# Kernel tuning notes

Hardware: AMD Instinct MI355X
Metric: run time of the kernel (lower is better)

The kernel has to match this reference:

```python
import jax, jax.numpy as jnp
import numpy as np

B, T, D = 4, 4096, 4096
G, C, K, M = 1, 4, 128, 32          # num_groups, n_splits, dw_hidden_dim, heads_per_group
I2 = 4                               # qkw inner dim = 2 * dynamic_hidden_dim (dyn_hidden = 32//16 = 2)
EPS = 1.1920929e-07                  # torch F.rms_norm default eps for fp32


def _rms_norm(x):
    # F.rms_norm over last dim, no learned scale
    return x * jax.lax.rsqrt(jnp.mean(x * x, axis=-1, keepdims=True) + EPS)


def setup_inputs() -> dict:
    key = jax.random.key(0)
    k0, k1, k2, k3 = jax.random.split(key, 4)
    dw1_std = np.sqrt(2.0 / (D + K))
    qkw_std = 0.02 / (np.sqrt(2 * 32 * 2) * (32 + 2))
    dd_std = 0.05 * np.sqrt(2.0 / (32 + D))
    return {
        "query_vec": jax.random.normal(k0, (B, T, D), dtype=jnp.float32),
        "dw1": jax.random.normal(k1, (D, G, C, K), dtype=jnp.float32) * dw1_std,
        "qkw": jax.random.normal(k2, (G, C, K, I2, M), dtype=jnp.float32) * qkw_std,
        "dd": jax.random.normal(k3, (D, G, M * C), dtype=jnp.float32) * dd_std,
        "norm_scale": jnp.ones((G,), dtype=jnp.float32) * 0.001,
    }


def reference(query_vec, dw1, qkw, dd, norm_scale):
    # dw_hidden: [B,T,G,C,K]
    dw_hidden = jnp.einsum('btd,dgck->btgck', query_vec, dw1)
    dw_hidden = jax.nn.gelu(dw_hidden, approximate=False)  # torch nn.GELU() is exact
    # w: [B,T,G,C,I2,M]
    w = jnp.einsum('btgck,gckim->btgcim', dw_hidden, qkw)
    half = qkw.shape[-2] // 2
    w1 = _rms_norm(w[..., :half, :])
    w2 = _rms_norm(w[..., half:, :]) * norm_scale  # norm_scale [G]=(1,) broadcasts over M
    # squeeze group dim (keep_group_dim=False) -> [B,T,C,I,M]
    w1 = w1[:, :, 0]
    w2 = w2[:, :, 0]
    # unbind along C: order pre_q, pre_k, post_q, post_k; key-wise pieces are discarded
    pre_qw1, post_qw1 = w1[:, :, 0], w1[:, :, 2]
    pre_qw2, post_qw2 = w2[:, :, 0], w2[:, :, 2]
    # dd: [B,T,G,M*C] -> tanh -> squeeze G -> split 4
    dd_out = jnp.tanh(jnp.einsum('btd,dgm->btgm', query_vec, dd))[:, :, 0]
    pre_qdd = dd_out[..., 0 * M:1 * M]
    post_qdd = dd_out[..., 2 * M:3 * M]
    # pack all live outputs into one array [B, T, 2*(2*I*M) + 2*M]
    flat = lambda a: a.reshape(a.shape[0], a.shape[1], -1)
    return jnp.concatenate(
        [flat(pre_qw1), flat(pre_qw2), pre_qdd,
         flat(post_qw1), flat(post_qw2), post_qdd], axis=-1)
```

## Files before the change

### kernel.cpp

```cpp
#include <hip/hip_runtime.h>
#include <cstdint>
#include <cstddef>

typedef __bf16 bf16x8 __attribute__((ext_vector_type(8)));
typedef float f32x4 __attribute__((ext_vector_type(4)));

#define D_DIM 4096
#define NCOL 320
#define BM 32
#define NKT 128
#define EPS_F 1.1920929e-07f
#define HS 136
#define STG 24576
#define RING 3
#define SMEM (RING * STG)

__device__ __forceinline__ void gld16(const void* g, void* l) {
  __builtin_amdgcn_global_load_lds(
      (const __attribute__((address_space(1))) unsigned int*)g,
      (__attribute__((address_space(3))) unsigned int*)l,
      16, 0, 0);
}

__global__ void dwp_pack(const float* __restrict__ dw1,
                         const float* __restrict__ qkw,
                         const float* __restrict__ dd,
                         __bf16* __restrict__ Wp,
                         __bf16* __restrict__ Qt) {
  const int b = blockIdx.x;
  const int t = threadIdx.x;
  if (b < 128) {
    __shared__ __bf16 tile[10240];
    const int kt = b;
    const int kk = t >> 3;
    const int d = kt * 32 + kk;
    const int u = kk >> 3;
#pragma unroll
    for (int j = 0; j < 5; ++j) {
      const int n0 = ((t & 7) + j * 8) * 8;
      const float* src;
      if (n0 < 128)      src = dw1 + (size_t)d * 512 + n0;
      else if (n0 < 256) src = dw1 + (size_t)d * 512 + 128 + n0;
      else if (n0 < 288) src = dd + (size_t)d * 128 + (n0 - 256);
      else               src = dd + (size_t)d * 128 + (n0 - 224);
      f32x4 v0 = *(const f32x4*)src;
      f32x4 v1 = *(const f32x4*)(src + 4);
#pragma unroll
      for (int q = 0; q < 8; ++q) {
        const int n = n0 + q;
        const int pos = n * 32 + ((u ^ ((n >> 1) & 3)) << 3) + (kk & 7);
        tile[pos] = (__bf16)((q < 4) ? v0[q] : v1[q - 4]);
      }
    }
    __syncthreads();
    __bf16* dst = Wp + (size_t)kt * 10240;
#pragma unroll
    for (int k = 0; k < 5; ++k) {
      const int u16 = t + k * 256;
      *(bf16x8*)(dst + u16 * 8) = *(const bf16x8*)(tile + u16 * 8);
    }
  } else {
#pragma unroll
    for (int ii = 0; ii < 16; ++ii) {
      const int q = t + ii * 256;
      const int c2 = q >> 11;
      const int rem = q & 2047;
      const int n = rem >> 4;
      const int k0 = (rem & 15) * 8;
      const float* src = qkw + (size_t)c2 * 32768 + (size_t)k0 * 128 + n;
      bf16x8 v;
#pragma unroll
      for (int j = 0; j < 8; ++j) v[j] = (__bf16)src[(size_t)j * 128];
      *(bf16x8*)(Qt + (size_t)c2 * 16384 + (size_t)n * 128 + k0) = v;
    }
  }
}

__global__ __launch_bounds__(256, 2) void dwp_main(
    const float* __restrict__ X,
    const __bf16* __restrict__ Wp,
    const __bf16* __restrict__ Qt,
    const float* __restrict__ NS,
    float* __restrict__ Out) {
  extern __shared__ __align__(16) unsigned char lds[];
  const int t = threadIdx.x;
  const int w = t >> 6;
  const int l = t & 63;
  const int lq = l >> 4;
  const int lm = l & 15;
  const int m0 = blockIdx.x * BM;

  const float* gA = X + (size_t)(m0 + (t >> 3)) * D_DIM +
                    (size_t)(((t & 7) ^ ((t >> 3) & 7)) * 4);

  const int cbase = w * 80;

  unsigned aoff0[2], aoff1[2], boff[5];
#pragma unroll
  for (int rt = 0; rt < 2; ++rt) {
    const int row = rt * 16 + lm;
    aoff0[rt] = (unsigned)(row * 128 + (((lq * 2 + 0) ^ (lm & 7)) * 16));
    aoff1[rt] = (unsigned)(row * 128 + (((lq * 2 + 1) ^ (lm & 7)) * 16));
  }
#pragma unroll
  for (int ct = 0; ct < 5; ++ct) {
    const int n = cbase + ct * 16 + lm;
    boff[ct] = (unsigned)(4096 + n * 64 + ((lq ^ ((n >> 1) & 3)) << 4));
  }

  f32x4 acc[2][5];
#pragma unroll
  for (int rt = 0; rt < 2; ++rt)
#pragma unroll
    for (int ct = 0; ct < 5; ++ct)
      acc[rt][ct] = (f32x4){0.f, 0.f, 0.f, 0.f};

  auto issue = [&](int kt, int slot) {
    unsigned char* base = lds + slot * STG;
    const __bf16* wsrc = Wp + (size_t)kt * 10240;
    gld16(gA + (size_t)kt * 32, base + w * 1024);
#pragma unroll
    for (int k = 0; k < 5; ++k)
      gld16(wsrc + (size_t)(k * 2048) + t * 8,
            base + 4096 + k * 4096 + w * 1024);
  };

  auto body = [&](int kt, int slot) {
    const unsigned char* cb = lds + slot * STG;
    bf16x8 a[2], b[5];
#pragma unroll
    for (int rt = 0; rt < 2; ++rt) {
      f32x4 x0 = *(const f32x4*)(cb + aoff0[rt]);
      f32x4 x1 = *(const f32x4*)(cb + aoff1[rt]);
#pragma unroll
      for (int j = 0; j < 4; ++j) {
        a[rt][j] = (__bf16)x0[j];
        a[rt][4 + j] = (__bf16)x1[j];
      }
    }
#pragma unroll
    for (int ct = 0; ct < 5; ++ct) b[ct] = *(const bf16x8*)(cb + boff[ct]);
#pragma unroll
    for (int rt = 0; rt < 2; ++rt)
#pragma unroll
      for (int ct = 0; ct < 5; ++ct)
        acc[rt][ct] =
            __builtin_amdgcn_mfma_f32_16x16x32_bf16(a[rt], b[ct], acc[rt][ct], 0, 0, 0);
  };

  issue(0, 0);
  issue(1, 1);

  int rb = 0;
  for (int kt = 0; kt < NKT - 1; ++kt) {
    asm volatile("s_waitcnt vmcnt(6)" ::: "memory");
    asm volatile("s_barrier" ::: "memory");
    if (kt + 2 < NKT) {
      int ri = rb + 2; if (ri >= RING) ri -= RING;
      issue(kt + 2, ri);
    }
    body(kt, rb);
    ++rb; if (rb == RING) rb = 0;
  }
  asm volatile("s_waitcnt vmcnt(0)" ::: "memory");
  asm volatile("s_barrier" ::: "memory");
  body(NKT - 1, rb);

  __syncthreads();

  const float ns = NS[0];

#pragma unroll
  for (int rt = 0; rt < 2; ++rt) {
#pragma unroll
    for (int ct = 0; ct < 5; ++ct) {
      const int ncol = cbase + ct * 16 + lm;
      const int rowb = rt * 16 + lq * 4;
      f32x4 v = acc[rt][ct];
      if (ncol < 256) {
        const int c2 = ncol >> 7;
        const int kcol = ncol & 127;
#pragma unroll
        for (int j = 0; j < 4; ++j) {
          float x = v[j];
          float g = 0.5f * x * (1.0f + erff(x * 0.70710678118f));
          *(__bf16*)(lds + (size_t)((c2 * 32 + rowb + j) * HS + kcol) * 2) = (__bf16)g;
        }
      } else {
        const int nd = ncol - 256;
        const int off = (nd < 32) ? (128 + nd) : (256 + nd);
#pragma unroll
        for (int j = 0; j < 4; ++j)
          Out[(size_t)(m0 + rowb + j) * NCOL + off] = tanhf(v[j]);
      }
    }
  }
  __syncthreads();

  const int c2b = w >> 1;
  const int nnb = (w & 1) * 64;
  f32x4 acc2[2][4];
#pragma unroll
  for (int rt = 0; rt < 2; ++rt)
#pragma unroll
    for (int ct = 0; ct < 4; ++ct) acc2[rt][ct] = (f32x4){0.f, 0.f, 0.f, 0.f};

#pragma unroll
  for (int ks = 0; ks < 4; ++ks) {
    bf16x8 a2[2], b2[4];
#pragma unroll
    for (int rt = 0; rt < 2; ++rt)
      a2[rt] = *(const bf16x8*)(lds +
               (size_t)((c2b * 32 + rt * 16 + lm) * HS + ks * 32 + lq * 8) * 2);
#pragma unroll
    for (int ct = 0; ct < 4; ++ct)
      b2[ct] = *(const bf16x8*)(Qt + (size_t)c2b * 16384 +
               (size_t)(nnb + ct * 16 + lm) * 128 + ks * 32 + lq * 8);
#pragma unroll
    for (int rt = 0; rt < 2; ++rt)
#pragma unroll
      for (int ct = 0; ct < 4; ++ct)
        acc2[rt][ct] =
            __builtin_amdgcn_mfma_f32_16x16x32_bf16(a2[rt], b2[ct], acc2[rt][ct], 0, 0, 0);
  }

#pragma unroll
  for (int rt = 0; rt < 2; ++rt) {
#pragma unroll
    for (int p = 0; p < 2; ++p) {
      const int i = (w & 1) * 2 + p;
      const float sce = (i >= 2) ? ns : 1.0f;
      f32x4 va = acc2[rt][2 * p];
      f32x4 vb = acc2[rt][2 * p + 1];
#pragma unroll
      for (int j = 0; j < 4; ++j) {
        float s = va[j] * va[j] + vb[j] * vb[j];
        s += __shfl_xor(s, 1);
        s += __shfl_xor(s, 2);
        s += __shfl_xor(s, 4);
        s += __shfl_xor(s, 8);
        const float sc = rsqrtf(s * (1.0f / 32.0f) + EPS_F) * sce;
        const size_t row = (size_t)(m0 + rt * 16 + lq * 4 + j);
        const int off = c2b * 160 + i * 32;
        Out[row * NCOL + off + lm] = va[j] * sc;
        Out[row * NCOL + off + 16 + lm] = vb[j] * sc;
      }
    }
  }
}

extern "C" void kernel_launch(void* const* d_in, const int* in_sizes, int n_in,
                              void* d_out, int out_size, void* d_ws, size_t ws_size,
                              hipStream_t stream) {
  const float* qv  = (const float*)d_in[0];
  const float* dw1 = (const float*)d_in[1];
  const float* qkw = (const float*)d_in[2];
  const float* dd  = (const float*)d_in[3];
  const float* ns  = (const float*)d_in[4];
  float* out = (float*)d_out;

  __bf16* Wp = (__bf16*)d_ws;
  __bf16* Qt = Wp + (size_t)4096 * 320;

  hipFuncSetAttribute((const void*)dwp_main,
                      hipFuncAttributeMaxDynamicSharedMemorySize, SMEM);

  dwp_pack<<<129, 256, 0, stream>>>(dw1, qkw, dd, Wp, Qt);
  dwp_main<<<512, 256, SMEM, stream>>>(qv, Wp, Qt, ns, out);
}
```

Measured before the change: 439.5 us.

## Split main kernel work across 8 waves per block instead of 4

Doubles the block to 512 threads, so each wave computes one 16-row by 80-column tile of the first GEMM instead of two row tiles. The global-to-LDS loads are redistributed so each wave issues three 16-byte loads per stage, and the vmcnt wait threshold is adjusted to match. The second GEMM and the RMS-norm epilogue are also split so each wave handles one output head block. This aims to raise the number of waves available to hide latency, at the cost of fewer MFMAs per LDS load and launch bounds that allow fewer registers per thread.

```diff
diff --git a/kernel.cpp b/kernel.cpp
--- a/kernel.cpp
+++ b/kernel.cpp
@@ -76,7 +76,7 @@
   }
 }
 
-__global__ __launch_bounds__(256, 2) void dwp_main(
+__global__ __launch_bounds__(512, 4) void dwp_main(
     const float* __restrict__ X,
     const __bf16* __restrict__ Wp,
     const __bf16* __restrict__ Qt,
@@ -90,17 +90,35 @@
   const int lm = l & 15;
   const int m0 = blockIdx.x * BM;
 
-  const float* gA = X + (size_t)(m0 + (t >> 3)) * D_DIM +
-                    (size_t)(((t & 7) ^ ((t >> 3) & 7)) * 4);
-
-  const int cbase = w * 80;
-
-  unsigned aoff0[2], aoff1[2], boff[5];
-#pragma unroll
-  for (int rt = 0; rt < 2; ++rt) {
-    const int row = rt * 16 + lm;
-    aoff0[rt] = (unsigned)(row * 128 + (((lq * 2 + 0) ^ (lm & 7)) * 16));
-    aoff1[rt] = (unsigned)(row * 128 + (((lq * 2 + 1) ^ (lm & 7)) * 16));
+  const int rg = w >> 2;
+  const int cg = w & 3;
+  const int cbase = cg * 80;
+
+  const char* gsrc[3];
+  int gstep[3];
+  unsigned ldsoff[3];
+#pragma unroll
+  for (int i = 0; i < 3; ++i) {
+    const int c = w * 3 + i;
+    if (c < 4) {
+      const int row = c * 8 + (l >> 3);
+      const int u = (l & 7) ^ (row & 7);
+      gsrc[i] = (const char*)(X + (size_t)(m0 + row) * D_DIM) + u * 16;
+      gstep[i] = 128;
+      ldsoff[i] = (unsigned)(c * 1024);
+    } else {
+      const int cb = c - 4;
+      gsrc[i] = (const char*)Wp + cb * 1024 + (size_t)l * 16;
+      gstep[i] = 20480;
+      ldsoff[i] = (unsigned)(4096 + cb * 1024);
+    }
+  }
+
+  unsigned aoff0, aoff1, boff[5];
+  {
+    const int row = rg * 16 + lm;
+    aoff0 = (unsigned)(row * 128 + (((lq * 2 + 0) ^ (lm & 7)) * 16));
+    aoff1 = (unsigned)(row * 128 + (((lq * 2 + 1) ^ (lm & 7)) * 16));
   }
 #pragma unroll
   for (int ct = 0; ct < 5; ++ct) {
@@ -108,44 +126,33 @@
     boff[ct] = (unsigned)(4096 + n * 64 + ((lq ^ ((n >> 1) & 3)) << 4));
   }
 
-  f32x4 acc[2][5];
-#pragma unroll
-  for (int rt = 0; rt < 2; ++rt)
-#pragma unroll
-    for (int ct = 0; ct < 5; ++ct)
-      acc[rt][ct] = (f32x4){0.f, 0.f, 0.f, 0.f};
+  f32x4 acc[5];
+#pragma unroll
+  for (int ct = 0; ct < 5; ++ct) acc[ct] = (f32x4){0.f, 0.f, 0.f, 0.f};
 
   auto issue = [&](int kt, int slot) {
     unsigned char* base = lds + slot * STG;
-    const __bf16* wsrc = Wp + (size_t)kt * 10240;
-    gld16(gA + (size_t)kt * 32, base + w * 1024);
-#pragma unroll
-    for (int k = 0; k < 5; ++k)
-      gld16(wsrc + (size_t)(k * 2048) + t * 8,
-            base + 4096 + k * 4096 + w * 1024);
+#pragma unroll
+    for (int i = 0; i < 3; ++i)
+      gld16(gsrc[i] + (size_t)kt * gstep[i], base + ldsoff[i]);
   };
 
   auto body = [&](int kt, int slot) {
     const unsigned char* cb = lds + slot * STG;
-    bf16x8 a[2], b[5];
-#pragma unroll
-    for (int rt = 0; rt < 2; ++rt) {
-      f32x4 x0 = *(const f32x4*)(cb + aoff0[rt]);
-      f32x4 x1 = *(const f32x4*)(cb + aoff1[rt]);
-#pragma unroll
-      for (int j = 0; j < 4; ++j) {
-        a[rt][j] = (__bf16)x0[j];
-        a[rt][4 + j] = (__bf16)x1[j];
-      }
+    bf16x8 a, b[5];
+    f32x4 x0 = *(const f32x4*)(cb + aoff0);
+    f32x4 x1 = *(const f32x4*)(cb + aoff1);
+#pragma unroll
+    for (int j = 0; j < 4; ++j) {
+      a[j] = (__bf16)x0[j];
+      a[4 + j] = (__bf16)x1[j];
     }
 #pragma unroll
     for (int ct = 0; ct < 5; ++ct) b[ct] = *(const bf16x8*)(cb + boff[ct]);
 #pragma unroll
-    for (int rt = 0; rt < 2; ++rt)
-#pragma unroll
-      for (int ct = 0; ct < 5; ++ct)
-        acc[rt][ct] =
-            __builtin_amdgcn_mfma_f32_16x16x32_bf16(a[rt], b[ct], acc[rt][ct], 0, 0, 0);
+    for (int ct = 0; ct < 5; ++ct)
+      acc[ct] =
+          __builtin_amdgcn_mfma_f32_16x16x32_bf16(a, b[ct], acc[ct], 0, 0, 0);
   };
 
   issue(0, 0);
@@ -153,7 +160,7 @@
 
   int rb = 0;
   for (int kt = 0; kt < NKT - 1; ++kt) {
-    asm volatile("s_waitcnt vmcnt(6)" ::: "memory");
+    asm volatile("s_waitcnt vmcnt(3)" ::: "memory");
     asm volatile("s_barrier" ::: "memory");
     if (kt + 2 < NKT) {
       int ri = rb + 2; if (ri >= RING) ri -= RING;
@@ -171,80 +178,74 @@
   const float ns = NS[0];
 
 #pragma unroll
-  for (int rt = 0; rt < 2; ++rt) {
-#pragma unroll
-    for (int ct = 0; ct < 5; ++ct) {
-      const int ncol = cbase + ct * 16 + lm;
-      const int rowb = rt * 16 + lq * 4;
-      f32x4 v = acc[rt][ct];
-      if (ncol < 256) {
-        const int c2 = ncol >> 7;
-        const int kcol = ncol & 127;
-#pragma unroll
-        for (int j = 0; j < 4; ++j) {
-          float x = v[j];
-          float g = 0.5f * x * (1.0f + erff(x * 0.70710678118f));
-          *(__bf16*)(lds + (size_t)((c2 * 32 + rowb + j) * HS + kcol) * 2) = (__bf16)g;
-        }
-      } else {
-        const int nd = ncol - 256;
-        const int off = (nd < 32) ? (128 + nd) : (256 + nd);
-#pragma unroll
-        for (int j = 0; j < 4; ++j)
-          Out[(size_t)(m0 + rowb + j) * NCOL + off] = tanhf(v[j]);
+  for (int ct = 0; ct < 5; ++ct) {
+    const int ncol = cbase + ct * 16 + lm;
+    const int rowb = rg * 16 + lq * 4;
+    f32x4 v = acc[ct];
+    if (ncol < 256) {
+      const int c2 = ncol >> 7;
+      const int kcol = ncol & 127;
+#pragma unroll
+      for (int j = 0; j < 4; ++j) {
+        float x = v[j];
+        float g = 0.5f * x * (1.0f + erff(x * 0.70710678118f));
+        *(__bf16*)(lds + (size_t)((c2 * 32 + rowb + j) * HS + kcol) * 2) = (__bf16)g;
       }
+    } else {
+      const int nd = ncol - 256;
+      const int off = (nd < 32) ? (128 + nd) : (256 + nd);
+#pragma unroll
+      for (int j = 0; j < 4; ++j)
+        Out[(size_t)(m0 + rowb + j) * NCOL + off] = tanhf(v[j]);
     }
   }
   __syncthreads();
 
-  const int c2b = w >> 1;
-  const int nnb = (w & 1) * 64;
-  f32x4 acc2[2][4];
+  const int c2b = w >> 2;
+  const int iq = w & 3;
+  const int nnb = iq * 32;
+  f32x4 acc2[2][2];
 #pragma unroll
   for (int rt = 0; rt < 2; ++rt)
 #pragma unroll
-    for (int ct = 0; ct < 4; ++ct) acc2[rt][ct] = (f32x4){0.f, 0.f, 0.f, 0.f};
+    for (int ct = 0; ct < 2; ++ct) acc2[rt][ct] = (f32x4){0.f, 0.f, 0.f, 0.f};
 
 #pragma unroll
   for (int ks = 0; ks < 4; ++ks) {
-    bf16x8 a2[2], b2[4];
+    bf16x8 a2[2], b2[2];
 #pragma unroll
     for (int rt = 0; rt < 2; ++rt)
       a2[rt] = *(const bf16x8*)(lds +
                (size_t)((c2b * 32 + rt * 16 + lm) * HS + ks * 32 + lq * 8) * 2);
 #pragma unroll
-    for (int ct = 0; ct < 4; ++ct)
+    for (int ct = 0; ct < 2; ++ct)
       b2[ct] = *(const bf16x8*)(Qt + (size_t)c2b * 16384 +
                (size_t)(nnb + ct * 16 + lm) * 128 + ks * 32 + lq * 8);
 #pragma unroll
     for (int rt = 0; rt < 2; ++rt)
 #pragma unroll
-      for (int ct = 0; ct < 4; ++ct)
+      for (int ct = 0; ct < 2; ++ct)
         acc2[rt][ct] =
             __builtin_amdgcn_mfma_f32_16x16x32_bf16(a2[rt], b2[ct], acc2[rt][ct], 0, 0, 0);
   }
 
+  const float sce = (iq >= 2) ? ns : 1.0f;
 #pragma unroll
   for (int rt = 0; rt < 2; ++rt) {
-#pragma unroll
-    for (int p = 0; p < 2; ++p) {
-      const int i = (w & 1) * 2 + p;
-      const float sce = (i >= 2) ? ns : 1.0f;
-      f32x4 va = acc2[rt][2 * p];
-      f32x4 vb = acc2[rt][2 * p + 1];
-#pragma unroll
-      for (int j = 0; j < 4; ++j) {
-        float s = va[j] * va[j] + vb[j] * vb[j];
-        s += __shfl_xor(s, 1);
-        s += __shfl_xor(s, 2);
-        s += __shfl_xor(s, 4);
-        s += __shfl_xor(s, 8);
-        const float sc = rsqrtf(s * (1.0f / 32.0f) + EPS_F) * sce;
-        const size_t row = (size_t)(m0 + rt * 16 + lq * 4 + j);
-        const int off = c2b * 160 + i * 32;
-        Out[row * NCOL + off + lm] = va[j] * sc;
-        Out[row * NCOL + off + 16 + lm] = vb[j] * sc;
-      }
+    f32x4 va = acc2[rt][0];
+    f32x4 vb = acc2[rt][1];
+#pragma unroll
+    for (int j = 0; j < 4; ++j) {
+      float s = va[j] * va[j] + vb[j] * vb[j];
+      s += __shfl_xor(s, 1);
+      s += __shfl_xor(s, 2);
+      s += __shfl_xor(s, 4);
+      s += __shfl_xor(s, 8);
+      const float sc = rsqrtf(s * (1.0f / 32.0f) + EPS_F) * sce;
+      const size_t row = (size_t)(m0 + rt * 16 + lq * 4 + j);
+      const int off = c2b * 160 + iq * 32;
+      Out[row * NCOL + off + lm] = va[j] * sc;
+      Out[row * NCOL + off + 16 + lm] = vb[j] * sc;
     }
   }
 }
@@ -266,5 +267,5 @@
                       hipFuncAttributeMaxDynamicSharedMemorySize, SMEM);
 
   dwp_pack<<<129, 256, 0, stream>>>(dw1, qkw, dd, Wp, Qt);
-  dwp_main<<<512, 256, SMEM, stream>>>(qv, Wp, Qt, ns, out);
-}
+  dwp_main<<<512, 512, SMEM, stream>>>(qv, Wp, Qt, ns, out);
+}
```

After: 443.8 us. Within noise of the previous version (+1.0%).
